# Performance work log

Hardware: AMD Instinct MI355X
Metric: run time of the kernel (lower is better)

Reference implementation:

```python
import jax, jax.numpy as jnp
import numpy as np

M = 2          # interp_dim
D = 4          # interp_degree
MESH_LOWER = np.array([0.0, 0.0], dtype=np.float32)
MESH_UPPER = np.array([1.0, 1.0], dtype=np.float32)
MESH_SIZE = np.array([64, 64], dtype=np.int32)   # coe grid = mesh_size*D+1 = [257, 257]


def _lagrange_basis(t):
    """t: [N, M] local coordinate in [0, D]; returns bases [N, M, D+1].
    L_j(t) = prod_{k != j} (t - k) / (j - k)."""
    ks = jnp.arange(D + 1, dtype=t.dtype)
    tk = t[..., None] - ks                       # [N, M, D+1]
    bs = []
    for j in range(D + 1):                       # small fixed loop over D+1=5 bases
        num = jnp.ones(t.shape, t.dtype)
        denom = 1.0
        for k in range(D + 1):
            if k != j:
                num = num * tk[..., k]
                denom *= float(j - k)
        bs.append(num / denom)
    return jnp.stack(bs, axis=-1)                # [N, M, D+1]


def setup_inputs() -> dict:
    key = jax.random.key(0)
    k1, k2 = jax.random.split(key)
    inputs = jax.random.uniform(k1, (2048, 2048, M), dtype=jnp.float32)  # points in [0,1)^2
    grid = tuple(int(s) * D + 1 for s in MESH_SIZE)                      # (257, 257)
    interp_coe = jax.random.normal(k2, grid, dtype=jnp.float32)
    return {"inputs": inputs, "interp_coe": interp_coe}


def reference(inputs, interp_coe):
    size = inputs.shape
    x = inputs.reshape(-1, M)                                   # [N, M]
    lower = jnp.asarray(MESH_LOWER, x.dtype)
    upper = jnp.asarray(MESH_UPPER, x.dtype)
    msize = jnp.asarray(MESH_SIZE.astype(np.float32), x.dtype)
    u = (x - lower) / (upper - lower) * msize                   # grid coordinates
    cell = jnp.clip(jnp.floor(u), 0.0, msize - 1.0)             # [N, M] element index
    t = (u - cell) * D                                          # local coord in [0, D]
    basis = _lagrange_basis(t)                                  # [N, M, D+1]
    base = cell.astype(jnp.int32) * D                           # [N, M] global node base index
    offs = jnp.arange(D + 1, dtype=jnp.int32)
    i0 = base[:, 0, None] + offs                                # [N, D+1]
    i1 = base[:, 1, None] + offs                                # [N, D+1]
    coe = interp_coe[i0[:, :, None], i1[:, None, :]]            # [N, D+1, D+1] gathered cell coes
    out = jnp.einsum('nij,ni,nj->n', coe, basis[:, 0], basis[:, 1])
    return out.reshape(size[:-1])
```

## Files before the change

### kernel.cpp

```cpp
#include <hip/hip_runtime.h>

#define NGRID 257
#define LDS_PITCH 260
#define LDS_BYTES (LDS_PITCH * NGRID * 2)
#define BLOCK 1024
#define GRID 256
#define ITERS 8

typedef _Float16 half4_t __attribute__((ext_vector_type(4)));

struct __attribute__((packed, aligned(4))) f4u { float x, y, z, w; };

__device__ __forceinline__ void lag_basis(float t, float b[5]) {
    float f0 = t;
    float f1 = t - 1.0f;
    float f2 = t - 2.0f;
    float f3 = t - 3.0f;
    float f4 = t - 4.0f;
    float p01 = f0 * f1;
    float p12 = f1 * f2;
    float p23 = f2 * f3;
    float p34 = f3 * f4;
    b[0] = p12 * p34 * (1.0f / 24.0f);
    b[1] = f0 * f2 * p34 * (-1.0f / 6.0f);
    b[2] = p01 * p34 * (1.0f / 4.0f);
    b[3] = p01 * f2 * f4 * (-1.0f / 6.0f);
    b[4] = p01 * p23 * (1.0f / 24.0f);
}

__device__ __forceinline__ float2 eval_pair(const _Float16* __restrict__ lds,
                                            float4 v) {
    float uA0 = v.x * 64.0f, uA1 = v.y * 64.0f;
    float uB0 = v.z * 64.0f, uB1 = v.w * 64.0f;
    float cA0 = fminf(fmaxf(floorf(uA0), 0.0f), 63.0f);
    float cA1 = fminf(fmaxf(floorf(uA1), 0.0f), 63.0f);
    float cB0 = fminf(fmaxf(floorf(uB0), 0.0f), 63.0f);
    float cB1 = fminf(fmaxf(floorf(uB1), 0.0f), 63.0f);
    float bA0[5], bA1[5], bB0[5], bB1[5];
    lag_basis((uA0 - cA0) * 4.0f, bA0);
    lag_basis((uA1 - cA1) * 4.0f, bA1);
    lag_basis((uB0 - cB0) * 4.0f, bB0);
    lag_basis((uB1 - cB1) * 4.0f, bB1);
    int offA = ((int)cA0 * 4) * LDS_PITCH + ((int)cA1 * 4);
    int offB = ((int)cB0 * 4) * LDS_PITCH + ((int)cB1 * 4);

    half4_t hA[5], hB[5];
    _Float16 eA[5], eB[5];
#pragma unroll
    for (int i = 0; i < 5; ++i) {
        const _Float16* rA = lds + offA + i * LDS_PITCH;
        const _Float16* rB = lds + offB + i * LDS_PITCH;
        hA[i] = *(const half4_t*)rA;
        hB[i] = *(const half4_t*)rB;
        eA[i] = rA[4];
        eB[i] = rB[4];
    }

    float accA = 0.0f, accB = 0.0f;
#pragma unroll
    for (int i = 0; i < 5; ++i) {
        float rdA = (float)hA[i][0] * bA1[0];
        rdA = fmaf((float)hA[i][1], bA1[1], rdA);
        rdA = fmaf((float)hA[i][2], bA1[2], rdA);
        rdA = fmaf((float)hA[i][3], bA1[3], rdA);
        rdA = fmaf((float)eA[i], bA1[4], rdA);
        accA = fmaf(bA0[i], rdA, accA);
        float rdB = (float)hB[i][0] * bB1[0];
        rdB = fmaf((float)hB[i][1], bB1[1], rdB);
        rdB = fmaf((float)hB[i][2], bB1[2], rdB);
        rdB = fmaf((float)hB[i][3], bB1[3], rdB);
        rdB = fmaf((float)eB[i], bB1[4], rdB);
        accB = fmaf(bB0[i], rdB, accB);
    }
    return make_float2(accA, accB);
}

__launch_bounds__(BLOCK)
__global__ void lagrange_kernel(const float* __restrict__ inputs,
                                const float* __restrict__ coe,
                                float* __restrict__ out,
                                int npairs) {
    extern __shared__ _Float16 lds[];

    for (int g = threadIdx.x; g < NGRID * 65; g += BLOCK) {
        int r = g / 65;
        int c4 = (g - r * 65) * 4;
        if (c4 < 256) {
            f4u q = *(const f4u*)(coe + r * NGRID + c4);
            half4_t h = { (_Float16)q.x, (_Float16)q.y,
                          (_Float16)q.z, (_Float16)q.w };
            *(half4_t*)(lds + r * LDS_PITCH + c4) = h;
        } else {
            lds[r * LDS_PITCH + 256] = (_Float16)coe[r * NGRID + 256];
        }
    }
    __syncthreads();

    const float4* __restrict__ in4 = (const float4*)inputs;
    float2* __restrict__ out2 = (float2*)out;
    const int tid = blockIdx.x * BLOCK + threadIdx.x;
    const int stride = GRID * BLOCK;

    float4 v[ITERS];
#pragma unroll
    for (int k = 0; k < ITERS; ++k) {
        int p = tid + k * stride;
        if (p < npairs) v[k] = in4[p];
    }
#pragma unroll
    for (int k = 0; k < ITERS; ++k) {
        int p = tid + k * stride;
        if (p < npairs) out2[p] = eval_pair(lds, v[k]);
    }
}

extern "C" void kernel_launch(void* const* d_in, const int* in_sizes, int n_in,
                              void* d_out, int out_size, void* d_ws, size_t ws_size,
                              hipStream_t stream) {
    const float* inputs = (const float*)d_in[0];
    const float* coe    = (const float*)d_in[1];
    float* out = (float*)d_out;
    int npairs = out_size >> 1;

    (void)hipFuncSetAttribute((const void*)lagrange_kernel,
                              hipFuncAttributeMaxDynamicSharedMemorySize,
                              LDS_BYTES);

    dim3 grid(GRID), block(BLOCK);
    hipLaunchKernelGGL(lagrange_kernel, grid, block, LDS_BYTES, stream,
                       inputs, coe, out, npairs);
}
```

Baseline: 100.4 us.

## Software-pipeline LDS gathers, use fdot2 for the inner dot, nontemporal stores

Restructures the main loop so the LDS gathers for the next pair are issued before the current pair is evaluated, double-buffering the fragments to hide LDS latency. Input loads now run two iterations ahead instead of all being issued up front. The inner row dot product uses fp16 fdot2 with basis weights rounded to half, and results are written with nontemporal stores under a launch-bounds occupancy hint. This drops the npairs bounds check, so correctness relies on the launch geometry covering the problem exactly, and rounding the basis to half adds precision error.

```diff
diff --git a/kernel.cpp b/kernel.cpp
--- a/kernel.cpp
+++ b/kernel.cpp
@@ -7,9 +7,16 @@
 #define GRID 256
 #define ITERS 8
 
+typedef _Float16 half2_t __attribute__((ext_vector_type(2)));
 typedef _Float16 half4_t __attribute__((ext_vector_type(4)));
+typedef float    f2v     __attribute__((ext_vector_type(2)));
 
 struct __attribute__((packed, aligned(4))) f4u { float x, y, z, w; };
+
+struct Frag {
+    half4_t hA[5], hB[5];
+    _Float16 eA[5], eB[5];
+};
 
 __device__ __forceinline__ void lag_basis(float t, float b[5]) {
     float f0 = t;
@@ -28,54 +35,65 @@
     b[4] = p01 * p23 * (1.0f / 24.0f);
 }
 
-__device__ __forceinline__ float2 eval_pair(const _Float16* __restrict__ lds,
-                                            float4 v) {
-    float uA0 = v.x * 64.0f, uA1 = v.y * 64.0f;
-    float uB0 = v.z * 64.0f, uB1 = v.w * 64.0f;
-    float cA0 = fminf(fmaxf(floorf(uA0), 0.0f), 63.0f);
-    float cA1 = fminf(fmaxf(floorf(uA1), 0.0f), 63.0f);
-    float cB0 = fminf(fmaxf(floorf(uB0), 0.0f), 63.0f);
-    float cB1 = fminf(fmaxf(floorf(uB1), 0.0f), 63.0f);
-    float bA0[5], bA1[5], bB0[5], bB1[5];
-    lag_basis((uA0 - cA0) * 4.0f, bA0);
-    lag_basis((uA1 - cA1) * 4.0f, bA1);
-    lag_basis((uB0 - cB0) * 4.0f, bB0);
-    lag_basis((uB1 - cB1) * 4.0f, bB1);
-    int offA = ((int)cA0 * 4) * LDS_PITCH + ((int)cA1 * 4);
-    int offB = ((int)cB0 * 4) * LDS_PITCH + ((int)cB1 * 4);
+__device__ __forceinline__ int pt_off(float x0, float x1) {
+    float u0 = x0 * 64.0f, u1 = x1 * 64.0f;
+    float c0 = fminf(fmaxf(floorf(u0), 0.0f), 63.0f);
+    float c1 = fminf(fmaxf(floorf(u1), 0.0f), 63.0f);
+    return ((int)c0 * 4) * LDS_PITCH + ((int)c1 * 4);
+}
 
-    half4_t hA[5], hB[5];
-    _Float16 eA[5], eB[5];
+__device__ __forceinline__ void stage_issue(const _Float16* __restrict__ lds,
+                                            float4 v, Frag& f) {
+    int offA = pt_off(v.x, v.y);
+    int offB = pt_off(v.z, v.w);
 #pragma unroll
     for (int i = 0; i < 5; ++i) {
         const _Float16* rA = lds + offA + i * LDS_PITCH;
         const _Float16* rB = lds + offB + i * LDS_PITCH;
-        hA[i] = *(const half4_t*)rA;
-        hB[i] = *(const half4_t*)rB;
-        eA[i] = rA[4];
-        eB[i] = rB[4];
+        f.hA[i] = *(const half4_t*)rA;
+        f.hB[i] = *(const half4_t*)rB;
+        f.eA[i] = rA[4];
+        f.eB[i] = rB[4];
     }
+}
 
-    float accA = 0.0f, accB = 0.0f;
+__device__ __forceinline__ float eval_from(const half4_t (&h)[5],
+                                           const _Float16 (&e)[5],
+                                           float x0, float x1) {
+    float u0 = x0 * 64.0f, u1 = x1 * 64.0f;
+    float c0 = fminf(fmaxf(floorf(u0), 0.0f), 63.0f);
+    float c1 = fminf(fmaxf(floorf(u1), 0.0f), 63.0f);
+    float b0[5], b1[5];
+    lag_basis((u0 - c0) * 4.0f, b0);
+    lag_basis((u1 - c1) * 4.0f, b1);
+    float acc = 0.0f;
+#if __has_builtin(__builtin_amdgcn_fdot2)
+    half2_t b01 = { (_Float16)b1[0], (_Float16)b1[1] };
+    half2_t b23 = { (_Float16)b1[2], (_Float16)b1[3] };
 #pragma unroll
     for (int i = 0; i < 5; ++i) {
-        float rdA = (float)hA[i][0] * bA1[0];
-        rdA = fmaf((float)hA[i][1], bA1[1], rdA);
-        rdA = fmaf((float)hA[i][2], bA1[2], rdA);
-        rdA = fmaf((float)hA[i][3], bA1[3], rdA);
-        rdA = fmaf((float)eA[i], bA1[4], rdA);
-        accA = fmaf(bA0[i], rdA, accA);
-        float rdB = (float)hB[i][0] * bB1[0];
-        rdB = fmaf((float)hB[i][1], bB1[1], rdB);
-        rdB = fmaf((float)hB[i][2], bB1[2], rdB);
-        rdB = fmaf((float)hB[i][3], bB1[3], rdB);
-        rdB = fmaf((float)eB[i], bB1[4], rdB);
-        accB = fmaf(bB0[i], rdB, accB);
+        half2_t lo = __builtin_shufflevector(h[i], h[i], 0, 1);
+        half2_t hi = __builtin_shufflevector(h[i], h[i], 2, 3);
+        float rd = (float)e[i] * b1[4];
+        rd = __builtin_amdgcn_fdot2(hi, b23, rd, false);
+        rd = __builtin_amdgcn_fdot2(lo, b01, rd, false);
+        acc = fmaf(b0[i], rd, acc);
     }
-    return make_float2(accA, accB);
+#else
+#pragma unroll
+    for (int i = 0; i < 5; ++i) {
+        float rd = (float)h[i][0] * b1[0];
+        rd = fmaf((float)h[i][1], b1[1], rd);
+        rd = fmaf((float)h[i][2], b1[2], rd);
+        rd = fmaf((float)h[i][3], b1[3], rd);
+        rd = fmaf((float)e[i], b1[4], rd);
+        acc = fmaf(b0[i], rd, acc);
+    }
+#endif
+    return acc;
 }
 
-__launch_bounds__(BLOCK)
+__launch_bounds__(BLOCK, 4)
 __global__ void lagrange_kernel(const float* __restrict__ inputs,
                                 const float* __restrict__ coe,
                                 float* __restrict__ out,
@@ -97,20 +115,27 @@
     __syncthreads();
 
     const float4* __restrict__ in4 = (const float4*)inputs;
-    float2* __restrict__ out2 = (float2*)out;
+    f2v* __restrict__ out2 = (f2v*)out;
     const int tid = blockIdx.x * BLOCK + threadIdx.x;
     const int stride = GRID * BLOCK;
+    (void)npairs;
 
     float4 v[ITERS];
+    Frag frag[2];
+
+    v[0] = in4[tid];
+    v[1] = in4[tid + stride];
+    stage_issue(lds, v[0], frag[0]);
+
 #pragma unroll
     for (int k = 0; k < ITERS; ++k) {
-        int p = tid + k * stride;
-        if (p < npairs) v[k] = in4[p];
-    }
-#pragma unroll
-    for (int k = 0; k < ITERS; ++k) {
-        int p = tid + k * stride;
-        if (p < npairs) out2[p] = eval_pair(lds, v[k]);
+        if (k + 2 < ITERS) v[k + 2] = in4[tid + (k + 2) * stride];
+        if (k + 1 < ITERS) stage_issue(lds, v[k + 1], frag[(k + 1) & 1]);
+        const Frag& f = frag[k & 1];
+        f2v r;
+        r.x = eval_from(f.hA, f.eA, v[k].x, v[k].y);
+        r.y = eval_from(f.hB, f.eB, v[k].z, v[k].w);
+        __builtin_nontemporal_store(r, &out2[tid + k * stride]);
     }
 }
 
```

After: 95.69 us. -4.7%, faster.
